# Performance work log

Measured on AMD Instinct MI355X. Metric: run time of the kernel, lower is better.

Reference implementation:

```python
import jax, jax.numpy as jnp
import numpy as np
from jax import lax

B, N, HID = 2, 1024, 2048
H, D, HKV = 32, 64, 8
GROUPS = H // HKV
CHUNK = 64
MAG = 0.5
GATE_NORM = 16.0


def setup_inputs() -> dict:
    key = jax.random.key(0)
    ks = jax.random.split(key, 5)
    hidden_states = jax.random.normal(ks[0], (B, N, HID), jnp.float32)
    Wq = jax.random.normal(ks[1], (HID, H * D), jnp.float32) * 0.02
    Wk = jax.random.normal(ks[2], (HID, HKV * D), jnp.float32) * 0.02
    Wv = jax.random.normal(ks[3], (HID, HKV * D), jnp.float32) * 0.02
    Wo = jax.random.normal(ks[4], (H * D, HID), jnp.float32) * 0.02
    return {"hidden_states": hidden_states, "Wq": Wq, "Wk": Wk, "Wv": Wv, "Wo": Wo}


def _repeat_kv(x, g):
    # [b, hkv, n, d] -> [b, hkv*g, n, d]
    return jnp.repeat(x, g, axis=1)


def _delta_rule_chunked(q, k, v, beta, chunk):
    """Chunked delta-rule linear attention (DeltaNet-style) with elementwise beta gate."""
    b, h, n, d = q.shape
    nc = n // chunk
    qc, kc, vc, bc = (x.reshape(b, h, nc, chunk, d) for x in (q, k, v, beta))
    k_beta = kc * bc
    v_beta = vc * bc
    # T = (I + tril(k_beta k^T, -1))^{-1}, a unit lower-triangular solve per chunk
    strict = jnp.tril(jnp.ones((chunk, chunk), bool), -1)
    L = jnp.einsum('bhnid,bhnjd->bhnij', k_beta, kc) * strict
    M = L + jnp.eye(chunk, dtype=q.dtype)
    eye = jnp.broadcast_to(jnp.eye(chunk, dtype=q.dtype), M.shape)
    T = jax.scipy.linalg.solve_triangular(M, eye, lower=True, unit_diagonal=True)
    u = jnp.einsum('bhnij,bhnjd->bhnid', T, v_beta)   # pseudo-values
    w = jnp.einsum('bhnij,bhnjd->bhnid', T, k_beta)   # pseudo-keys
    causal = jnp.tril(jnp.ones((chunk, chunk), bool))

    def step(S, xs):
        qi, ki, ui, wi = xs  # each [b, h, chunk, d]; S: [b, h, d, d]
        u_p = ui - jnp.einsum('bhcd,bhde->bhce', wi, S)
        attn = jnp.einsum('bhid,bhjd->bhij', qi, ki) * causal
        o = jnp.einsum('bhcd,bhde->bhce', qi, S) + jnp.einsum('bhij,bhjd->bhid', attn, u_p)
        S_new = S + jnp.einsum('bhcd,bhce->bhde', ki, u_p)
        return S_new, o

    xs = tuple(jnp.moveaxis(x, 2, 0) for x in (qc, kc, u, w))  # [nc, b, h, chunk, d]
    S0 = jnp.zeros((b, h, d, d), q.dtype)
    S_final, o = lax.scan(step, S0, xs)
    o = jnp.moveaxis(o, 0, 2).reshape(b, h, n, d)
    return o, S_final


def reference(hidden_states, Wq, Wk, Wv, Wo):
    b, n, _ = hidden_states.shape
    q = hidden_states @ Wq            # [b, n, H*D]
    k = hidden_states @ Wk            # [b, n, HKV*D]
    v = hidden_states @ Wv            # [b, n, HKV*D]
    g = k  # AdaptiveAvgPool1d(512 -> 512) is the identity here

    qh = q.reshape(b, n, H, D).transpose(0, 2, 1, 3)      # [b, H, n, D]
    kh = k.reshape(b, n, HKV, D).transpose(0, 2, 1, 3)    # [b, HKV, n, D]
    vh = v.reshape(b, n, HKV, D).transpose(0, 2, 1, 3)
    gh = g.reshape(b, n, HKV, D).transpose(0, 2, 1, 3)
    k_rep = _repeat_kv(kh, GROUPS)
    v_rep = _repeat_kv(vh, GROUPS)
    g_rep = _repeat_kv(gh, GROUPS)

    # linear-attention branch: softmax feature maps + log-sigmoid gate
    ql = jax.nn.softmax(qh, axis=-1).astype(jnp.float32)
    kl = jax.nn.softmax(k_rep, axis=-1).astype(jnp.float32)
    gl = (jax.nn.log_sigmoid(g_rep) / GATE_NORM).astype(jnp.float32)
    o_lin, _ = _delta_rule_chunked(ql, kl, v_rep.astype(jnp.float32), gl, CHUNK)
    o_lin = o_lin.transpose(0, 2, 1, 3).reshape(b, n, H * D) @ Wo

    # base (vanilla causal) attention branch
    scale = 1.0 / np.sqrt(D).astype(np.float32)
    scores = jnp.einsum('bhid,bhjd->bhij', qh, k_rep) * scale
    causal = jnp.tril(jnp.ones((n, n), bool))
    scores = jnp.where(causal, scores, jnp.finfo(scores.dtype).min)
    attn_weights = jax.nn.softmax(scores, axis=-1)
    o_base = jnp.einsum('bhij,bhjd->bhid', attn_weights, v_rep)
    o_base = o_base.transpose(0, 2, 1, 3).reshape(b, n, H * D) @ Wo

    out = MAG * o_lin + (1.0 - MAG) * o_base
    return out, attn_weights
```

## Files before the change

kernel.cpp:

```cpp
#include <hip/hip_runtime.h>
#include <hip/hip_bf16.h>

constexpr int Bc = 2, Nc = 1024, HIDc = 2048, Hc = 32, Dc = 64, HKVc = 8, NCc = 16;

typedef unsigned short bfu;
typedef __attribute__((ext_vector_type(8))) short frag_ab;
typedef __attribute__((ext_vector_type(4))) float frag_cd;

__device__ __forceinline__ bfu f2bf(float f) {
  unsigned int u = __float_as_uint(f);
  unsigned int r = u + 0x7fffu + ((u >> 16) & 1u);
  return (bfu)(r >> 16);
}
__device__ __forceinline__ ushort4 pack4(float4 v) {
  ushort4 r; r.x = f2bf(v.x); r.y = f2bf(v.y); r.z = f2bf(v.z); r.w = f2bf(v.w);
  return r;
}

__device__ __forceinline__ void gl16(const bfu* g, bfu* l) {
  __builtin_amdgcn_global_load_lds(
      (const __attribute__((address_space(1))) void*)g,
      (__attribute__((address_space(3))) void*)l, 16, 0, 0);
}

__global__ __launch_bounds__(256) void cast_bf16_k(
    const float* __restrict__ in, bfu* __restrict__ out)
{
  const size_t i = ((size_t)blockIdx.x * 256 + threadIdx.x) * 4;
  *(ushort4*)(out + i) = pack4(*(const float4*)(in + i));
}

__global__ __launch_bounds__(256) void transpose_cast_k(
    const float* __restrict__ W, bfu* __restrict__ WT, int K, int N)
{
  __shared__ float t[32][33];
  const int bn = blockIdx.x * 32, bk = blockIdx.y * 32;
  const int x = threadIdx.x & 31, y = threadIdx.x >> 5;
#pragma unroll
  for (int i = 0; i < 32; i += 8)
    t[y + i][x] = W[(size_t)(bk + y + i) * N + bn + x];
  __syncthreads();
#pragma unroll
  for (int i = 0; i < 32; i += 8)
    WT[(size_t)(bn + y + i) * K + bk + x] = f2bf(t[x][y + i]);
}

__global__ __launch_bounds__(256) void transpose_v_k(
    const float* __restrict__ v, bfu* __restrict__ vt)
{
  __shared__ __align__(16) bfu T[64][72];
  const int blk = blockIdx.x;
  const int nt = blk & 15, bh = blk >> 4;
  const int hk = bh & 7, b = bh >> 3;
  const int tid = threadIdx.x;
  const int n = tid >> 2, dv0 = (tid & 3) * 16;
  const float* src = v + ((size_t)(b * Nc + nt * 64 + n) * 8 + hk) * 64 + dv0;
#pragma unroll
  for (int e = 0; e < 16; ++e) T[dv0 + e][n] = f2bf(src[e]);
  __syncthreads();
  const int r = tid >> 3, c = (tid & 7) * 8;
#pragma unroll
  for (int hh = 0; hh < 2; ++hh) {
    const int dv = r + hh * 32;
    *(uint4*)(vt + ((size_t)(bh * 64 + dv)) * 1024 + nt * 64 + c) =
        *(const uint4*)&T[dv][c];
  }
}

__device__ __forceinline__ void gemm128_gl(
    const bfu* __restrict__ A, const bfu* __restrict__ BT,
    float* __restrict__ C, const int Nn, const int m0, const int n0,
    bfu* As, bfu* Bs)
{
  const int tid = threadIdx.x;
  const int wave = tid >> 6, lane = tid & 63;
  const int wm = (wave >> 1) * 64, wn = (wave & 1) * 64;
  const int fm = lane & 15, quad = lane >> 4;
  const int sr = tid >> 2, skc = (tid & 3) * 8;

  frag_cd acc[4][4];
#pragma unroll
  for (int i = 0; i < 4; ++i)
#pragma unroll
    for (int j = 0; j < 4; ++j) acc[i][j] = (frag_cd){0.f, 0.f, 0.f, 0.f};

  const bfu* Ag = A + (size_t)(m0 + sr) * 2048 + skc;
  const bfu* Bg = BT + (size_t)(n0 + sr) * 2048 + skc;
  bfu* Al = As + tid * 8;
  bfu* Bl = Bs + tid * 8;

  for (int k0 = 0; k0 < 2048; k0 += 32) {
    gl16(Ag + k0, Al);
    gl16(Ag + k0 + (size_t)64 * 2048, Al + 64 * 32);
    gl16(Bg + k0, Bl);
    gl16(Bg + k0 + (size_t)64 * 2048, Bl + 64 * 32);
    __syncthreads();
    frag_ab a[4], b[4];
#pragma unroll
    for (int im = 0; im < 4; ++im)
      a[im] = *(const frag_ab*)&As[(size_t)(wm + im * 16 + fm) * 32 + quad * 8];
#pragma unroll
    for (int in = 0; in < 4; ++in)
      b[in] = *(const frag_ab*)&Bs[(size_t)(wn + in * 16 + fm) * 32 + quad * 8];
#pragma unroll
    for (int im = 0; im < 4; ++im)
#pragma unroll
      for (int in = 0; in < 4; ++in)
        acc[im][in] = __builtin_amdgcn_mfma_f32_16x16x32_bf16(
            a[im], b[in], acc[im][in], 0, 0, 0);
    __syncthreads();
  }
#pragma unroll
  for (int im = 0; im < 4; ++im)
#pragma unroll
    for (int in = 0; in < 4; ++in) {
      const int n = n0 + wn + in * 16 + fm;
#pragma unroll
      for (int r = 0; r < 4; ++r) {
        const int m = m0 + wm + im * 16 + quad * 4 + r;
        C[(size_t)m * Nn + n] = acc[im][in][r];
      }
    }
}

__global__ __launch_bounds__(256) void gemm_qkv_k(
    const bfu* __restrict__ A, const bfu* __restrict__ BTq,
    const bfu* __restrict__ BTk, const bfu* __restrict__ BTv,
    float* __restrict__ Cq, float* __restrict__ Ck, float* __restrict__ Cv)
{
  __shared__ __align__(16) bfu As[128 * 32];
  __shared__ __align__(16) bfu Bs[128 * 32];
  int bx = blockIdx.x;
  const bfu* BT; float* C; int Nn;
  if (bx < 16)      { BT = BTq; C = Cq; Nn = 2048; }
  else if (bx < 20) { BT = BTk; C = Ck; Nn = 512; bx -= 16; }
  else              { BT = BTv; C = Cv; Nn = 512; bx -= 20; }
  gemm128_gl(A, BT, C, Nn, blockIdx.y * 128, bx * 128, As, Bs);
}

__global__ __launch_bounds__(256) void gemm_wo_k(
    const bfu* __restrict__ A, const bfu* __restrict__ BT, float* __restrict__ C)
{
  __shared__ __align__(16) bfu As[128 * 32];
  __shared__ __align__(16) bfu Bs[128 * 32];
  gemm128_gl(A, BT, C, 2048, blockIdx.y * 128, blockIdx.x * 128, As, Bs);
}

__global__ __launch_bounds__(256) void gates64_k(
    const float* __restrict__ kin, float* __restrict__ kl, float* __restrict__ gl,
    bfu* __restrict__ k_bf)
{
  const int r = blockIdx.x * 4 + (threadIdx.x >> 6);
  const int lane = threadIdx.x & 63;
  const size_t idx = (size_t)r * 64 + lane;
  const float x = kin[idx];
  k_bf[idx] = f2bf(x);
  float m = x;
#pragma unroll
  for (int o = 32; o > 0; o >>= 1) m = fmaxf(m, __shfl_xor(m, o, 64));
  const float e = __expf(x - m);
  float s = e;
#pragma unroll
  for (int o = 32; o > 0; o >>= 1) s += __shfl_xor(s, o, 64);
  kl[idx] = e / s;
  const float ls = fminf(x, 0.f) - log1pf(__expf(-fabsf(x)));
  gl[idx] = ls * 0.0625f;
}

__global__ __launch_bounds__(256) void chunk_prep_k(
    const float* __restrict__ kl, const float* __restrict__ v,
    const float* __restrict__ gl, float* __restrict__ u_out, float* __restrict__ w_out)
{
  __shared__ __align__(16) float KC[64][68];
  __shared__ float KB[64][65];
  __shared__ float VB[64][65];
  const int blk = blockIdx.x;
  const int c = blk & 15, bh = blk >> 4;
  const int hk = bh & 7, b = bh >> 3;
  const int tid = threadIdx.x;
  for (int x = tid; x < 4096; x += 256) {
    const int i = x >> 6, d = x & 63;
    const size_t src = ((size_t)(b * Nc + c * 64 + i) * 8 + hk) * 64 + d;
    const float kv = kl[src], g = gl[src], vv = v[src];
    KC[d][i] = kv; KB[i][d] = kv * g; VB[i][d] = vv * g;
  }
  __syncthreads();
  const int li = tid >> 2, j0 = (tid & 3) * 16;
  float acc[16];
#pragma unroll
  for (int jj = 0; jj < 16; ++jj) acc[jj] = 0.f;
  for (int d = 0; d < 64; ++d) {
    const float kb = KB[li][d];
    const float4 c0v = *(const float4*)&KC[d][j0];
    const float4 c1v = *(const float4*)&KC[d][j0 + 4];
    const float4 c2v = *(const float4*)&KC[d][j0 + 8];
    const float4 c3v = *(const float4*)&KC[d][j0 + 12];
    acc[0] += kb * c0v.x;  acc[1] += kb * c0v.y;  acc[2] += kb * c0v.z;  acc[3] += kb * c0v.w;
    acc[4] += kb * c1v.x;  acc[5] += kb * c1v.y;  acc[6] += kb * c1v.z;  acc[7] += kb * c1v.w;
    acc[8] += kb * c2v.x;  acc[9] += kb * c2v.y;  acc[10] += kb * c2v.z; acc[11] += kb * c2v.w;
    acc[12] += kb * c3v.x; acc[13] += kb * c3v.y; acc[14] += kb * c3v.z; acc[15] += kb * c3v.w;
  }
  __syncthreads();
#pragma unroll
  for (int jj = 0; jj < 16; ++jj)
    KC[li][j0 + jj] = (j0 + jj < li) ? acc[jj] : 0.f;
  __syncthreads();
  for (int r0 = 0; r0 < 64; r0 += 16) {
    if (r0 > 0) {
      for (int p = tid; p < 2048; p += 256) {
        const int ii = p >> 7, dc = p & 127;
        float (*X)[65] = (dc < 64) ? VB : KB;
        const int d = dc & 63;
        float a2 = X[r0 + ii][d];
        for (int j = 0; j < r0; ++j) a2 -= KC[r0 + ii][j] * X[j][d];
        X[r0 + ii][d] = a2;
      }
      __syncthreads();
    }
    if (tid < 128) {
      const int d = tid & 63;
      float (*X)[65] = (tid < 64) ? VB : KB;
      for (int i = r0 + 1; i < r0 + 16; ++i) {
        float a2 = X[i][d];
        for (int j = r0; j < i; ++j) a2 -= KC[i][j] * X[j][d];
        X[i][d] = a2;
      }
    }
    __syncthreads();
  }
  for (int x = tid; x < 4096; x += 256) {
    u_out[(size_t)blk * 4096 + x] = VB[x >> 6][x & 63];
    w_out[(size_t)blk * 4096 + x] = KB[x >> 6][x & 63];
  }
}

__global__ __launch_bounds__(256) void scan_k(
    const float* __restrict__ u_ps, const float* __restrict__ w_ps,
    const float* __restrict__ kl, float* __restrict__ u_p, float* __restrict__ S_pre)
{
  __shared__ __align__(16) float S[64][20];
  __shared__ __align__(16) float up[64][20];
  __shared__ __align__(16) float kw[64][68];
  __shared__ __align__(16) float kt[64][68];
  const int blk = blockIdx.x;
  const int cg = blk & 3;
  const int bh = blk >> 2;
  const int hk = bh & 7, b = bh >> 3;
  const int t = threadIdx.x;
  const int row = t >> 2;
  const int c0 = (t & 3) * 4;
  const int cbase = cg * 16;
  for (int x = t; x < 1024; x += 256) S[x >> 4][x & 15] = 0.f;
  __syncthreads();
  for (int c = 0; c < 16; ++c) {
    const size_t cb = ((size_t)bh * 16 + c) * 4096;
    const float4 upre = *(const float4*)(u_ps + cb + row * 64 + cbase + c0);
    for (int x = t; x < 1024; x += 256) {
      const int i = x >> 4, d4 = (x & 15) * 4;
      *(float4*)&kw[i][d4] = *(const float4*)(w_ps + cb + i * 64 + d4);
      *(float4*)&kt[i][d4] =
          *(const float4*)(kl + ((size_t)(b * Nc + c * 64 + i) * 8 + hk) * 64 + d4);
    }
    for (int x = t; x < 1024; x += 256) {
      const int i = x >> 4, cc = x & 15;
      S_pre[cb + i * 64 + cbase + cc] = S[i][cc];
    }
    __syncthreads();
    {
      float a0 = upre.x, a1 = upre.y, a2 = upre.z, a3 = upre.w;
      for (int e4 = 0; e4 < 64; e4 += 4) {
        const float4 wv4 = *(const float4*)&kw[row][e4];
#pragma unroll
        for (int ee = 0; ee < 4; ++ee) {
          const float wv = ((const float*)&wv4)[ee];
          const float4 sv = *(const float4*)&S[e4 + ee][c0];
          a0 -= wv * sv.x; a1 -= wv * sv.y; a2 -= wv * sv.z; a3 -= wv * sv.w;
        }
      }
      const float4 o = make_float4(a0, a1, a2, a3);
      *(float4*)&up[row][c0] = o;
      *(float4*)(u_p + cb + row * 64 + cbase + c0) = o;
    }
    __syncthreads();
    {
      const float4 sv = *(const float4*)&S[row][c0];
      float s0 = sv.x, s1 = sv.y, s2 = sv.z, s3 = sv.w;
      for (int i = 0; i < 64; ++i) {
        const float kv = kt[i][row];
        const float4 uv = *(const float4*)&up[i][c0];
        s0 += kv * uv.x; s1 += kv * uv.y; s2 += kv * uv.z; s3 += kv * uv.w;
      }
      *(float4*)&S[row][c0] = make_float4(s0, s1, s2, s3);
    }
    __syncthreads();
  }
}

__global__ __launch_bounds__(256) void olin_k(
    const float* __restrict__ qraw, const float* __restrict__ kl,
    const float* __restrict__ upb, const float* __restrict__ S_pre,
    float* __restrict__ o_comb, bfu* __restrict__ q_bf)
{
  __shared__ float Q[64][65];
  __shared__ __align__(16) float Bb[64][68];
  __shared__ float At[64][65];
  const int blk = blockIdx.x;
  const int c = blk & 15, bh = blk >> 4;
  const int h = bh & 31, b = bh >> 5, hk = h >> 2;
  const int tid = threadIdx.x;
  const int i = tid >> 2, d0 = (tid & 3) * 16;
  for (int x = tid; x < 4096; x += 256) {
    const int r = x >> 6, d = x & 63;
    const size_t qidx = ((size_t)(b * Nc + c * 64 + r) * 32 + h) * 64 + d;
    const float qv = qraw[qidx];
    Q[r][d] = qv;
    q_bf[qidx] = f2bf(qv);
    Bb[d][r] = kl[((size_t)(b * Nc + c * 64 + r) * 8 + hk) * 64 + d];
  }
  __syncthreads();
  {
    float mx = -1e30f;
#pragma unroll
    for (int j = 0; j < 16; ++j) mx = fmaxf(mx, Q[i][d0 + j]);
#pragma unroll
    for (int o = 1; o < 4; o <<= 1) mx = fmaxf(mx, __shfl_xor(mx, o, 64));
    float ev[16];
    float sum = 0.f;
#pragma unroll
    for (int j = 0; j < 16; ++j) { ev[j] = __expf(Q[i][d0 + j] - mx); sum += ev[j]; }
#pragma unroll
    for (int o = 1; o < 4; o <<= 1) sum += __shfl_xor(sum, o, 64);
    const float inv = 1.f / sum;
#pragma unroll
    for (int j = 0; j < 16; ++j) Q[i][d0 + j] = ev[j] * inv;
  }
  __syncthreads();
  {
    float a[16];
#pragma unroll
    for (int j = 0; j < 16; ++j) a[j] = 0.f;
    for (int d = 0; d < 64; ++d) {
      const float qv = Q[i][d];
      const float4 b0 = *(const float4*)&Bb[d][d0];
      const float4 b1 = *(const float4*)&Bb[d][d0 + 4];
      const float4 b2 = *(const float4*)&Bb[d][d0 + 8];
      const float4 b3 = *(const float4*)&Bb[d][d0 + 12];
      a[0] += qv * b0.x;  a[1] += qv * b0.y;  a[2] += qv * b0.z;  a[3] += qv * b0.w;
      a[4] += qv * b1.x;  a[5] += qv * b1.y;  a[6] += qv * b1.z;  a[7] += qv * b1.w;
      a[8] += qv * b2.x;  a[9] += qv * b2.y;  a[10] += qv * b2.z; a[11] += qv * b2.w;
      a[12] += qv * b3.x; a[13] += qv * b3.y; a[14] += qv * b3.z; a[15] += qv * b3.w;
    }
#pragma unroll
    for (int j = 0; j < 16; ++j) At[i][d0 + j] = (d0 + j <= i) ? a[j] : 0.f;
  }
  __syncthreads();
  const size_t cb = ((size_t)(b * 8 + hk) * 16 + c) * 4096;
  for (int x = tid; x < 4096; x += 256) Bb[x >> 6][x & 63] = S_pre[cb + x];
  __syncthreads();
  float o[16];
#pragma unroll
  for (int j = 0; j < 16; ++j) o[j] = 0.f;
  for (int e = 0; e < 64; ++e) {
    const float qv = Q[i][e];
    const float4 b0 = *(const float4*)&Bb[e][d0];
    const float4 b1 = *(const float4*)&Bb[e][d0 + 4];
    const float4 b2 = *(const float4*)&Bb[e][d0 + 8];
    const float4 b3 = *(const float4*)&Bb[e][d0 + 12];
    o[0] += qv * b0.x;  o[1] += qv * b0.y;  o[2] += qv * b0.z;  o[3] += qv * b0.w;
    o[4] += qv * b1.x;  o[5] += qv * b1.y;  o[6] += qv * b1.z;  o[7] += qv * b1.w;
    o[8] += qv * b2.x;  o[9] += qv * b2.y;  o[10] += qv * b2.z; o[11] += qv * b2.w;
    o[12] += qv * b3.x; o[13] += qv * b3.y; o[14] += qv * b3.z; o[15] += qv * b3.w;
  }
  __syncthreads();
  for (int x = tid; x < 4096; x += 256) Bb[x >> 6][x & 63] = upb[cb + x];
  __syncthreads();
  for (int j2 = 0; j2 < 64; ++j2) {
    const float av = At[i][j2];
    const float4 b0 = *(const float4*)&Bb[j2][d0];
    const float4 b1 = *(const float4*)&Bb[j2][d0 + 4];
    const float4 b2 = *(const float4*)&Bb[j2][d0 + 8];
    const float4 b3 = *(const float4*)&Bb[j2][d0 + 12];
    o[0] += av * b0.x;  o[1] += av * b0.y;  o[2] += av * b0.z;  o[3] += av * b0.w;
    o[4] += av * b1.x;  o[5] += av * b1.y;  o[6] += av * b1.z;  o[7] += av * b1.w;
    o[8] += av * b2.x;  o[9] += av * b2.y;  o[10] += av * b2.z; o[11] += av * b2.w;
    o[12] += av * b3.x; o[13] += av * b3.y; o[14] += av * b3.z; o[15] += av * b3.w;
  }
  float* oc = o_comb + ((size_t)(b * Nc + c * 64 + i) * 32 + h) * 64 + d0;
#pragma unroll
  for (int j = 0; j < 16; ++j) oc[j] = 0.5f * o[j];
}

template <int LDK>
__device__ __forceinline__ void stage_tile(
    const bfu* __restrict__ g, size_t row_stride, bfu* dst, int tid)
{
  const int xr = tid >> 3;
  const int xc = (tid & 7) * 8;
#pragma unroll
  for (int hh = 0; hh < 2; ++hh) {
    const int row = xr + hh * 32;
    *(uint4*)&dst[(size_t)row * LDK + xc] =
        *(const uint4*)(g + (size_t)row * row_stride + xc);
  }
}

__global__ __launch_bounds__(256) void attn_mfma_k(
    const bfu* __restrict__ qbf, const bfu* __restrict__ kbf,
    const bfu* __restrict__ vtbf, float* __restrict__ attn,
    const float* __restrict__ o_comb, bfu* __restrict__ oc_bf)
{
  constexpr int LDK = 72;
  __shared__ __align__(16) bfu Qt[64 * LDK];
  __shared__ __align__(16) bfu Kt[64 * LDK];
  __shared__ __align__(16) bfu Vt[64 * LDK];
  __shared__ __align__(16) bfu Pmat[64 * LDK];
  __shared__ float mred[4][64];
  __shared__ float lred[4][64];
  __shared__ float mfin[64];
  __shared__ float lfin[64];
  const int blk = blockIdx.x;
  const int ib = blk & 15, bh = blk >> 4;
  const int h = bh & 31, b = bh >> 5, hk = h >> 2;
  const int tid = threadIdx.x;
  const int wave = tid >> 6, lane = tid & 63;
  const int fm = lane & 15, quad = lane >> 4;
  const int wj = wave * 16;
  const int im0 = wave * 16;

  stage_tile<LDK>(qbf + ((size_t)(b * Nc + ib * 64) * 32 + h) * 64,
                  (size_t)32 * 64, Qt, tid);
  __syncthreads();
  frag_ab qb[4][2];
#pragma unroll
  for (int in = 0; in < 4; ++in)
#pragma unroll
    for (int kk = 0; kk < 2; ++kk)
      qb[in][kk] = *(const frag_ab*)&Qt[(size_t)(in * 16 + fm) * LDK + kk * 32 + quad * 8];

  float m[4], l[4];
#pragma unroll
  for (int in = 0; in < 4; ++in) { m[in] = -1e30f; l[in] = 0.f; }

  for (int jt = 0; jt <= ib; ++jt) {
    __syncthreads();
    stage_tile<LDK>(kbf + ((size_t)(b * Nc + jt * 64) * 8 + hk) * 64,
                    (size_t)8 * 64, Kt, tid);
    __syncthreads();
    frag_ab ka[2];
    ka[0] = *(const frag_ab*)&Kt[(size_t)(wj + fm) * LDK + quad * 8];
    ka[1] = *(const frag_ab*)&Kt[(size_t)(wj + fm) * LDK + 32 + quad * 8];
    const bool diag = (jt == ib);
#pragma unroll
    for (int in = 0; in < 4; ++in) {
      frag_cd acc = (frag_cd){0.f, 0.f, 0.f, 0.f};
      acc = __builtin_amdgcn_mfma_f32_16x16x32_bf16(ka[0], qb[in][0], acc, 0, 0, 0);
      acc = __builtin_amdgcn_mfma_f32_16x16x32_bf16(ka[1], qb[in][1], acc, 0, 0, 0);
      const int iloc = in * 16 + fm;
      float sv[4];
      bool vd[4];
      float tm = -1e30f;
#pragma unroll
      for (int r = 0; r < 4; ++r) {
        const int jloc = wj + quad * 4 + r;
        vd[r] = !diag || (jloc <= iloc);
        sv[r] = acc[r] * 0.125f;
        if (vd[r]) tm = fmaxf(tm, sv[r]);
      }
      const float mn = fmaxf(m[in], tm);
      float lsum = 0.f;
#pragma unroll
      for (int r = 0; r < 4; ++r)
        if (vd[r]) lsum += __expf(sv[r] - mn);
      l[in] = l[in] * __expf(m[in] - mn) + lsum;
      m[in] = mn;
    }
  }
#pragma unroll
  for (int in = 0; in < 4; ++in) {
    float mm = m[in], ll = l[in];
#pragma unroll
    for (int off = 16; off < 64; off <<= 1) {
      const float mo = __shfl_xor(mm, off, 64);
      const float lo = __shfl_xor(ll, off, 64);
      const float mn = fmaxf(mm, mo);
      ll = ll * __expf(mm - mn) + lo * __expf(mo - mn);
      mm = mn;
    }
    if (quad == 0) { mred[wave][in * 16 + fm] = mm; lred[wave][in * 16 + fm] = ll; }
  }
  __syncthreads();
  if (tid < 64) {
    float M = -1e30f;
#pragma unroll
    for (int w = 0; w < 4; ++w) M = fmaxf(M, mred[w][tid]);
    float L = 0.f;
#pragma unroll
    for (int w = 0; w < 4; ++w) L += lred[w][tid] * __expf(mred[w][tid] - M);
    mfin[tid] = M;
    lfin[tid] = L;
  }
  __syncthreads();
  float mi[4], il[4];
#pragma unroll
  for (int in = 0; in < 4; ++in) {
    mi[in] = mfin[in * 16 + fm];
    il[in] = 1.f / lfin[in * 16 + fm];
  }

  float* arow0 = attn + ((size_t)(b * 32 + h) * 1024 + ib * 64) * 1024;
  frag_cd o[4];
#pragma unroll
  for (int in = 0; in < 4; ++in) o[in] = (frag_cd){0.f, 0.f, 0.f, 0.f};

  for (int jt = 0; jt <= ib; ++jt) {
    __syncthreads();
    stage_tile<LDK>(kbf + ((size_t)(b * Nc + jt * 64) * 8 + hk) * 64,
                    (size_t)8 * 64, Kt, tid);
    stage_tile<LDK>(vtbf + (size_t)(b * 8 + hk) * 64 * 1024 + jt * 64,
                    (size_t)1024, Vt, tid);
    __syncthreads();
    frag_ab ka[2];
    ka[0] = *(const frag_ab*)&Kt[(size_t)(wj + fm) * LDK + quad * 8];
    ka[1] = *(const frag_ab*)&Kt[(size_t)(wj + fm) * LDK + 32 + quad * 8];
    const bool diag = (jt == ib);
#pragma unroll
    for (int in = 0; in < 4; ++in) {
      frag_cd acc = (frag_cd){0.f, 0.f, 0.f, 0.f};
      acc = __builtin_amdgcn_mfma_f32_16x16x32_bf16(ka[0], qb[in][0], acc, 0, 0, 0);
      acc = __builtin_amdgcn_mfma_f32_16x16x32_bf16(ka[1], qb[in][1], acc, 0, 0, 0);
      const int iloc = in * 16 + fm;
      float p[4];
#pragma unroll
      for (int r = 0; r < 4; ++r) {
        const int jloc = wj + quad * 4 + r;
        const bool vdr = !diag || (jloc <= iloc);
        p[r] = vdr ? __expf(acc[r] * 0.125f - mi[in]) * il[in] : 0.f;
      }
      *(float4*)(arow0 + (size_t)iloc * 1024 + jt * 64 + wj + quad * 4) =
          make_float4(p[0], p[1], p[2], p[3]);
      ushort4 w;
      w.x = f2bf(p[0]); w.y = f2bf(p[1]); w.z = f2bf(p[2]); w.w = f2bf(p[3]);
      *(ushort4*)&Pmat[(size_t)iloc * LDK + wj + quad * 4] = w;
    }
    __syncthreads();
    frag_ab pa[2];
    pa[0] = *(const frag_ab*)&Pmat[(size_t)(im0 + fm) * LDK + quad * 8];
    pa[1] = *(const frag_ab*)&Pmat[(size_t)(im0 + fm) * LDK + 32 + quad * 8];
#pragma unroll
    for (int in = 0; in < 4; ++in) {
      frag_ab vb0 = *(const frag_ab*)&Vt[(size_t)(in * 16 + fm) * LDK + quad * 8];
      frag_ab vb1 = *(const frag_ab*)&Vt[(size_t)(in * 16 + fm) * LDK + 32 + quad * 8];
      o[in] = __builtin_amdgcn_mfma_f32_16x16x32_bf16(pa[0], vb0, o[in], 0, 0, 0);
      o[in] = __builtin_amdgcn_mfma_f32_16x16x32_bf16(pa[1], vb1, o[in], 0, 0, 0);
    }
  }
  for (int jt2 = ib + 1; jt2 < 16; ++jt2) {
    const float4 z = make_float4(0.f, 0.f, 0.f, 0.f);
    for (int x = tid; x < 1024; x += 256) {
      const int row = x >> 4, c4 = (x & 15) * 4;
      *(float4*)(arow0 + (size_t)row * 1024 + jt2 * 64 + c4) = z;
    }
  }
#pragma unroll
  for (int in = 0; in < 4; ++in)
#pragma unroll
    for (int r = 0; r < 4; ++r) {
      const int i = im0 + quad * 4 + r;
      const size_t idx = ((size_t)(b * Nc + ib * 64 + i) * 32 + h) * 64 + in * 16 + fm;
      oc_bf[idx] = f2bf(o_comb[idx] + 0.5f * o[in][r]);
    }
}

extern "C" void kernel_launch(void* const* d_in, const int* in_sizes, int n_in,
                              void* d_out, int out_size, void* d_ws, size_t ws_size,
                              hipStream_t stream) {
  const float* hs = (const float*)d_in[0];
  const float* Wq = (const float*)d_in[1];
  const float* Wk = (const float*)d_in[2];
  const float* Wv = (const float*)d_in[3];
  const float* Wo = (const float*)d_in[4];
  float* out = (float*)d_out;
  float* attn = out + (size_t)Bc * Nc * HIDc;

  float* ws = (float*)d_ws;
  float* q_raw  = ws;
  float* k_raw  = q_raw + 4194304;
  float* v_raw  = k_raw + 1048576;
  float* kl     = v_raw + 1048576;
  float* gl     = kl + 1048576;
  float* u_ps   = gl + 1048576;
  float* w_ps   = u_ps + 2097152;
  float* upb    = w_ps + 2097152;
  float* S_pre  = upb + 2097152;
  float* o_comb = S_pre + 2097152;
  float* mbuf   = o_comb + 4194304;
  float* lbuf   = mbuf + 65536;
  bfu* bstart = (bfu*)(lbuf + 65536);
  bfu* hs_bf  = bstart;
  bfu* WqT    = hs_bf + 4194304;
  bfu* WkT    = WqT + 4194304;
  bfu* WvT    = WkT + 1048576;
  bfu* WoT    = WvT + 1048576;
  bfu* oc_bf  = WoT + 4194304;
  bfu* q_bf   = hs_bf;
  bfu* k_bf   = WqT;
  bfu* vt_bf  = WqT + 1048576;

  cast_bf16_k<<<4096, 256, 0, stream>>>(hs, hs_bf);
  transpose_cast_k<<<dim3(64, 64), 256, 0, stream>>>(Wq, WqT, 2048, 2048);
  transpose_cast_k<<<dim3(16, 64), 256, 0, stream>>>(Wk, WkT, 2048, 512);
  transpose_cast_k<<<dim3(16, 64), 256, 0, stream>>>(Wv, WvT, 2048, 512);
  transpose_cast_k<<<dim3(64, 64), 256, 0, stream>>>(Wo, WoT, 2048, 2048);
  gemm_qkv_k<<<dim3(24, 16), 256, 0, stream>>>(hs_bf, WqT, WkT, WvT,
                                               q_raw, k_raw, v_raw);
  gates64_k<<<4096, 256, 0, stream>>>(k_raw, kl, gl, k_bf);
  transpose_v_k<<<256, 256, 0, stream>>>(v_raw, vt_bf);
  chunk_prep_k<<<256, 256, 0, stream>>>(kl, v_raw, gl, u_ps, w_ps);
  scan_k<<<64, 256, 0, stream>>>(u_ps, w_ps, kl, upb, S_pre);
  olin_k<<<1024, 256, 0, stream>>>(q_raw, kl, upb, S_pre, o_comb, q_bf);
  attn_mfma_k<<<1024, 256, 0, stream>>>(q_bf, k_bf, vt_bf, attn, o_comb, oc_bf);
  gemm_wo_k<<<dim3(16, 16), 256, 0, stream>>>(oc_bf, WoT, out);
}
```

Baseline: 650.9 us.

## Merge prep kernels and stage attention probabilities through LDS for coalesced writes

Folds the hidden-state cast and the four weight transpose-casts into one launch that dispatches on block index, removing four kernel launches. In the attention kernel, probability tiles are first written to a padded fp32 LDS buffer and then stored to the global attention matrix with row-contiguous float4 writes instead of scattered per-fragment stores. Q fragments are now loaded straight from global memory rather than staged through LDS, which drops one barrier. The cost is extra LDS (about 17KB more) and an additional LDS round trip per tile, which may lower occupancy.

```diff
diff --git a/kernel.cpp b/kernel.cpp
--- a/kernel.cpp
+++ b/kernel.cpp
@@ -23,18 +23,27 @@
       (__attribute__((address_space(3))) void*)l, 16, 0, 0);
 }
 
-__global__ __launch_bounds__(256) void cast_bf16_k(
-    const float* __restrict__ in, bfu* __restrict__ out)
-{
-  const size_t i = ((size_t)blockIdx.x * 256 + threadIdx.x) * 4;
-  *(ushort4*)(out + i) = pack4(*(const float4*)(in + i));
-}
-
-__global__ __launch_bounds__(256) void transpose_cast_k(
-    const float* __restrict__ W, bfu* __restrict__ WT, int K, int N)
+__global__ __launch_bounds__(256) void prep_k(
+    const float* __restrict__ hs, bfu* __restrict__ hs_bf,
+    const float* __restrict__ Wq, bfu* __restrict__ WqT,
+    const float* __restrict__ Wk, bfu* __restrict__ WkT,
+    const float* __restrict__ Wv, bfu* __restrict__ WvT,
+    const float* __restrict__ Wo, bfu* __restrict__ WoT)
 {
   __shared__ float t[32][33];
-  const int bn = blockIdx.x * 32, bk = blockIdx.y * 32;
+  int bx = blockIdx.x;
+  if (bx < 4096) {
+    const size_t i = ((size_t)bx * 256 + threadIdx.x) * 4;
+    *(ushort4*)(hs_bf + i) = pack4(*(const float4*)(hs + i));
+    return;
+  }
+  bx -= 4096;
+  const float* W; bfu* WT; int K, N, nb;
+  if (bx < 4096)      { W = Wq; WT = WqT; K = 2048; N = 2048; nb = 64; }
+  else if (bx < 5120) { W = Wk; WT = WkT; K = 2048; N = 512;  nb = 16; bx -= 4096; }
+  else if (bx < 6144) { W = Wv; WT = WvT; K = 2048; N = 512;  nb = 16; bx -= 5120; }
+  else                { W = Wo; WT = WoT; K = 2048; N = 2048; nb = 64; bx -= 6144; }
+  const int bn = (bx % nb) * 32, bk = (bx / nb) * 32;
   const int x = threadIdx.x & 31, y = threadIdx.x >> 5;
 #pragma unroll
   for (int i = 0; i < 32; i += 8)
@@ -410,10 +419,10 @@
     const float* __restrict__ o_comb, bfu* __restrict__ oc_bf)
 {
   constexpr int LDK = 72;
-  __shared__ __align__(16) bfu Qt[64 * LDK];
   __shared__ __align__(16) bfu Kt[64 * LDK];
   __shared__ __align__(16) bfu Vt[64 * LDK];
   __shared__ __align__(16) bfu Pmat[64 * LDK];
+  __shared__ __align__(16) float Pf[64][68];
   __shared__ float mred[4][64];
   __shared__ float lred[4][64];
   __shared__ float mfin[64];
@@ -427,15 +436,13 @@
   const int wj = wave * 16;
   const int im0 = wave * 16;
 
-  stage_tile<LDK>(qbf + ((size_t)(b * Nc + ib * 64) * 32 + h) * 64,
-                  (size_t)32 * 64, Qt, tid);
-  __syncthreads();
   frag_ab qb[4][2];
 #pragma unroll
   for (int in = 0; in < 4; ++in)
 #pragma unroll
     for (int kk = 0; kk < 2; ++kk)
-      qb[in][kk] = *(const frag_ab*)&Qt[(size_t)(in * 16 + fm) * LDK + kk * 32 + quad * 8];
+      qb[in][kk] = *(const frag_ab*)(qbf +
+          ((size_t)(b * Nc + ib * 64 + in * 16 + fm) * 32 + h) * 64 + kk * 32 + quad * 8);
 
   float m[4], l[4];
 #pragma unroll
@@ -536,13 +543,17 @@
         const bool vdr = !diag || (jloc <= iloc);
         p[r] = vdr ? __expf(acc[r] * 0.125f - mi[in]) * il[in] : 0.f;
       }
-      *(float4*)(arow0 + (size_t)iloc * 1024 + jt * 64 + wj + quad * 4) =
-          make_float4(p[0], p[1], p[2], p[3]);
+      *(float4*)&Pf[iloc][wj + quad * 4] = make_float4(p[0], p[1], p[2], p[3]);
       ushort4 w;
       w.x = f2bf(p[0]); w.y = f2bf(p[1]); w.z = f2bf(p[2]); w.w = f2bf(p[3]);
       *(ushort4*)&Pmat[(size_t)iloc * LDK + wj + quad * 4] = w;
     }
     __syncthreads();
+    for (int x = tid; x < 1024; x += 256) {
+      const int row = x >> 4, c4 = (x & 15) * 4;
+      *(float4*)(arow0 + (size_t)row * 1024 + jt * 64 + c4) =
+          *(const float4*)&Pf[row][c4];
+    }
     frag_ab pa[2];
     pa[0] = *(const frag_ab*)&Pmat[(size_t)(im0 + fm) * LDK + quad * 8];
     pa[1] = *(const frag_ab*)&Pmat[(size_t)(im0 + fm) * LDK + 32 + quad * 8];
@@ -606,11 +617,8 @@
   bfu* k_bf   = WqT;
   bfu* vt_bf  = WqT + 1048576;
 
-  cast_bf16_k<<<4096, 256, 0, stream>>>(hs, hs_bf);
-  transpose_cast_k<<<dim3(64, 64), 256, 0, stream>>>(Wq, WqT, 2048, 2048);
-  transpose_cast_k<<<dim3(16, 64), 256, 0, stream>>>(Wk, WkT, 2048, 512);
-  transpose_cast_k<<<dim3(16, 64), 256, 0, stream>>>(Wv, WvT, 2048, 512);
-  transpose_cast_k<<<dim3(64, 64), 256, 0, stream>>>(Wo, WoT, 2048, 2048);
+  prep_k<<<14336, 256, 0, stream>>>(hs, hs_bf, Wq, WqT, Wk, WkT,
+                                    Wv, WvT, Wo, WoT);
   gemm_qkv_k<<<dim3(24, 16), 256, 0, stream>>>(hs_bf, WqT, WkT, WvT,
                                                q_raw, k_raw, v_raw);
   gates64_k<<<4096, 256, 0, stream>>>(k_raw, kl, gl, k_bf);
```

Result: faster. 636.2 us (-2.3%).
